# Kernel tuning notes

Hardware: AMD Instinct MI355X
Metric: run time of the kernel (lower is better)

The kernel has to match this reference:

```python
import jax, jax.numpy as jnp
import numpy as np

H = 16
D_MODEL = 1024
D_K = D_MODEL // H


def setup_inputs() -> dict:
    key = jax.random.key(0)
    ks = jax.random.split(key, 11)
    B, S = 4, 2048
    scale = 1.0 / np.sqrt(D_MODEL)
    inp = {
        "query": jax.random.normal(ks[0], (B, S, D_MODEL), dtype=jnp.float32),
        "key": jax.random.normal(ks[1], (B, S, D_MODEL), dtype=jnp.float32),
        "value": jax.random.normal(ks[2], (B, S, D_MODEL), dtype=jnp.float32),
        "Wq": jax.random.normal(ks[3], (D_MODEL, D_MODEL), dtype=jnp.float32) * scale,
        "bq": jnp.zeros((D_MODEL,), dtype=jnp.float32),
        "Wk": jax.random.normal(ks[4], (D_MODEL, D_MODEL), dtype=jnp.float32) * scale,
        "bk": jnp.zeros((D_MODEL,), dtype=jnp.float32),
        "Wv": jax.random.normal(ks[5], (D_MODEL, D_MODEL), dtype=jnp.float32) * scale,
        "bv": jnp.zeros((D_MODEL,), dtype=jnp.float32),
        "Wo": jax.random.normal(ks[6], (D_MODEL, D_MODEL), dtype=jnp.float32) * scale,
        "bo": jnp.zeros((D_MODEL,), dtype=jnp.float32),
    }
    return inp


def reference(query, key, value, Wq, bq, Wk, bk, Wv, bv, Wo, bo):
    B, S, _ = query.shape

    def proj(x, W, b):
        # nn.Linear: x @ W.T + b, then split heads -> [B, H, S, D_K]
        y = jnp.einsum("bsd,ed->bse", x, W) + b
        return y.reshape(B, S, H, D_K).transpose(0, 2, 1, 3)

    q = proj(query, Wq, bq)
    k = proj(key, Wk, bk)
    v = proj(value, Wv, bv)

    scores = jnp.einsum("bhqd,bhkd->bhqk", q, k) / jnp.sqrt(jnp.float32(D_K))
    attn = jax.nn.softmax(scores, axis=-1)
    out = jnp.einsum("bhqk,bhkd->bhqd", attn, v)  # [B,H,S,D_K]
    out = out.transpose(0, 2, 1, 3).reshape(B, S, H * D_K)
    # final linear (dropout disabled in eval / deterministic reference)
    return jnp.einsum("bsd,ed->bse", out, Wo) + bo
```

## Files before the change

kernel.cpp:

```cpp
#include <hip/hip_runtime.h>
#include <stdint.h>

typedef __attribute__((ext_vector_type(8))) short short8;
typedef __attribute__((ext_vector_type(4))) float floatx4;

#define DEV __device__ __forceinline__

DEV unsigned short f2bf(float x) {
  unsigned u = __float_as_uint(x);
  u += 0x7fffu + ((u >> 16) & 1u);
  return (unsigned short)(u >> 16);
}

DEV unsigned pkbf(float hi, float lo) {
  return __builtin_amdgcn_perm(__float_as_uint(hi) + 0x8000u,
                               __float_as_uint(lo) + 0x8000u, 0x07060302u);
}

DEV void load_lds16(const unsigned short* g, unsigned short* l) {
  __builtin_amdgcn_global_load_lds(
      (const __attribute__((address_space(1))) void*)g,
      (__attribute__((address_space(3))) void*)l, 16, 0, 0);
}

DEV void lds_fence() { asm volatile("" ::: "memory"); }

__global__ void cvt_all(const float* __restrict__ Wq, const float* __restrict__ Wk,
                        const float* __restrict__ Wv, const float* __restrict__ Wo,
                        const float* __restrict__ Xq, const float* __restrict__ Xk,
                        const float* __restrict__ Xv,
                        unsigned short* __restrict__ Wb, unsigned short* __restrict__ XqB,
                        unsigned short* __restrict__ XkB, unsigned short* __restrict__ XvB) {
  int bid = blockIdx.x;
  const float* src;
  unsigned short* dst;
  int off;
  if (bid < 4096) {
    int sel = bid >> 10;
    src = sel == 0 ? Wq : sel == 1 ? Wk : sel == 2 ? Wv : Wo;
    dst = Wb + (size_t)sel * 1048576;
    off = bid & 1023;
  } else {
    bid -= 4096;
    int sel = bid >> 13;
    src = sel == 0 ? Xq : sel == 1 ? Xk : Xv;
    dst = sel == 0 ? XqB : sel == 1 ? XkB : XvB;
    off = bid & 8191;
  }
  int i = (off * 256 + threadIdx.x) * 4;
  float4 v = *(const float4*)(src + i);
  uint2 o;
  o.x = pkbf(v.y, v.x);
  o.y = pkbf(v.w, v.z);
  *(uint2*)(dst + i) = o;
}

#define SCQ (0.125f * 1.44269504089f)
__global__ __launch_bounds__(256, 2) void qkv_gemm(
    const unsigned short* __restrict__ XqB, const unsigned short* __restrict__ XkB,
    const unsigned short* __restrict__ XvB,
    const unsigned short* __restrict__ Wb,
    const float* __restrict__ bq, const float* __restrict__ bk, const float* __restrict__ bv,
    unsigned short* __restrict__ Qp, unsigned short* __restrict__ Kp,
    unsigned short* __restrict__ VTp) {
  __shared__ alignas(16) unsigned short Xs[128 * 32];
  __shared__ alignas(16) unsigned short Ws[128 * 32];
  const int z = blockIdx.z;
  const unsigned short* X = z == 0 ? XqB : z == 1 ? XkB : XvB;
  const unsigned short* W = Wb + (size_t)z * 1048576;
  const float* bias = z == 0 ? bq : z == 1 ? bk : bv;

  const int tid = threadIdx.x;
  const int lane = tid & 63, wave = tid >> 6;
  const int lcol = lane & 15, quad = lane >> 4;
  const int wo = blockIdx.x * 128;
  const int xo = blockIdx.y * 128;
  const int wm = (wave & 1) * 64;
  const int wn = (wave >> 1) * 64;

  floatx4 acc[4][4];
  for (int mi = 0; mi < 4; ++mi)
    for (int ni = 0; ni < 4; ++ni)
      for (int r = 0; r < 4; ++r) acc[mi][ni][r] = 0.f;

  const unsigned short* Abuf = (z < 2) ? Xs : Ws;
  const unsigned short* Bbuf = (z < 2) ? Ws : Xs;

  for (int kt = 0; kt < 32; ++kt) {
    const int k0 = kt * 32;
    int c = tid;
    load_lds16(W + (size_t)(wo + (c >> 2)) * 1024 + k0 + (c & 3) * 8, Ws + c * 8);
    load_lds16(X + (size_t)(xo + (c >> 2)) * 1024 + k0 + (c & 3) * 8, Xs + c * 8);
    c = tid + 256;
    load_lds16(W + (size_t)(wo + (c >> 2)) * 1024 + k0 + (c & 3) * 8, Ws + c * 8);
    load_lds16(X + (size_t)(xo + (c >> 2)) * 1024 + k0 + (c & 3) * 8, Xs + c * 8);
    __syncthreads();
    short8 af[4], bf[4];
#pragma unroll
    for (int mi = 0; mi < 4; ++mi)
      af[mi] = *(const short8*)(Abuf + (wm + mi * 16 + lcol) * 32 + quad * 8);
#pragma unroll
    for (int ni = 0; ni < 4; ++ni)
      bf[ni] = *(const short8*)(Bbuf + (wn + ni * 16 + lcol) * 32 + quad * 8);
#pragma unroll
    for (int mi = 0; mi < 4; ++mi)
#pragma unroll
      for (int ni = 0; ni < 4; ++ni)
        acc[mi][ni] = __builtin_amdgcn_mfma_f32_16x16x32_bf16(af[mi], bf[ni], acc[mi][ni], 0, 0, 0);
    __syncthreads();
  }

  if (z < 2) {
    unsigned short* Out = z == 0 ? Qp : Kp;
    const float scl = z == 0 ? SCQ : 1.f;
#pragma unroll
    for (int ni = 0; ni < 4; ++ni) {
      int col = wo + wn + ni * 16 + lcol;
      float bvx = bias[col];
      int h = col >> 6, d = col & 63;
#pragma unroll
      for (int mi = 0; mi < 4; ++mi) {
        int rbase = xo + wm + mi * 16 + quad * 4;
#pragma unroll
        for (int r = 0; r < 4; ++r) {
          int grow = rbase + r;
          int bb = grow >> 11, s = grow & 2047;
          Out[((size_t)(bb * 16 + h) * 2048 + s) * 64 + d] = f2bf((acc[mi][ni][r] + bvx) * scl);
        }
      }
    }
  } else {
#pragma unroll
    for (int mi = 0; mi < 4; ++mi) {
      int dbase = wo + wm + mi * 16 + quad * 4;
#pragma unroll
      for (int r = 0; r < 4; ++r) {
        int dg = dbase + r;
        float bvx = bias[dg];
        int h = dg >> 6, dk = dg & 63;
#pragma unroll
        for (int ni = 0; ni < 4; ++ni) {
          int sg = xo + wn + ni * 16 + lcol;
          int bb = sg >> 11, ss = sg & 2047;
          VTp[((size_t)(bb * 16 + h) * 64 + dk) * 2048 + ss] = f2bf(acc[mi][ni][r] + bvx);
        }
      }
    }
  }
}

__global__ __launch_bounds__(256, 2) void gemm_o(
    const unsigned short* __restrict__ A, const unsigned short* __restrict__ Bw,
    const float* __restrict__ bias, float* __restrict__ Out) {
  __shared__ alignas(16) unsigned short As[128 * 32];
  __shared__ alignas(16) unsigned short Bs[128 * 32];
  const int tid = threadIdx.x;
  const int lane = tid & 63, wave = tid >> 6;
  const int lcol = lane & 15, quad = lane >> 4;
  const int n0 = blockIdx.x * 128;
  const int m0 = blockIdx.y * 128;
  const int wm = (wave & 1) * 64;
  const int wn = (wave >> 1) * 64;

  floatx4 acc[4][4];
  for (int mi = 0; mi < 4; ++mi)
    for (int ni = 0; ni < 4; ++ni)
      for (int r = 0; r < 4; ++r) acc[mi][ni][r] = 0.f;

  for (int kt = 0; kt < 32; ++kt) {
    const int k0 = kt * 32;
    int c = tid;
    load_lds16(Bw + (size_t)(n0 + (c >> 2)) * 1024 + k0 + (c & 3) * 8, Bs + c * 8);
    load_lds16(A  + (size_t)(m0 + (c >> 2)) * 1024 + k0 + (c & 3) * 8, As + c * 8);
    c = tid + 256;
    load_lds16(Bw + (size_t)(n0 + (c >> 2)) * 1024 + k0 + (c & 3) * 8, Bs + c * 8);
    load_lds16(A  + (size_t)(m0 + (c >> 2)) * 1024 + k0 + (c & 3) * 8, As + c * 8);
    __syncthreads();
    short8 af[4], bf[4];
#pragma unroll
    for (int mi = 0; mi < 4; ++mi)
      af[mi] = *(const short8*)(As + (wm + mi * 16 + lcol) * 32 + quad * 8);
#pragma unroll
    for (int ni = 0; ni < 4; ++ni)
      bf[ni] = *(const short8*)(Bs + (wn + ni * 16 + lcol) * 32 + quad * 8);
#pragma unroll
    for (int mi = 0; mi < 4; ++mi)
#pragma unroll
      for (int ni = 0; ni < 4; ++ni)
        acc[mi][ni] = __builtin_amdgcn_mfma_f32_16x16x32_bf16(af[mi], bf[ni], acc[mi][ni], 0, 0, 0);
    __syncthreads();
  }
#pragma unroll
  for (int ni = 0; ni < 4; ++ni) {
    int col = n0 + wn + ni * 16 + lcol;
    float bv = bias[col];
#pragma unroll
    for (int mi = 0; mi < 4; ++mi) {
      int rbase = m0 + wm + mi * 16 + quad * 4;
#pragma unroll
      for (int r = 0; r < 4; ++r)
        Out[(size_t)(rbase + r) * 1024 + col] = acc[mi][ni][r] + bv;
    }
  }
}

__global__ __launch_bounds__(256, 2) void attn_kernel(
    const unsigned short* __restrict__ Qp, const unsigned short* __restrict__ Kp,
    const unsigned short* __restrict__ VTp, unsigned short* __restrict__ Ctx) {
  __shared__ alignas(16) unsigned short Ks[128 * 64];
  __shared__ alignas(16) unsigned short Vt[64 * 128];

  const int tid = threadIdx.x;
  const int lane = tid & 63, wave = tid >> 6;
  const int lcol = lane & 15, quad = lane >> 4;
  const int wq = wave * 32;
  const int qt = blockIdx.x, h = blockIdx.y, b = blockIdx.z;
  const size_t bh = (size_t)(b * 16 + h) * 2048 * 64;
  const unsigned short* Qb = Qp + bh + (size_t)qt * 128 * 64;
  const unsigned short* Kb = Kp + bh;
  const unsigned short* VTb = VTp + (size_t)(b * 16 + h) * 64 * 2048;

#pragma unroll
  for (int i = 0; i < 4; ++i) {
    int p = tid + i * 256;
    int row = p >> 3, pj = p & 7;
    load_lds16(Qb + row * 64 + ((pj ^ (row & 7)) * 8), Ks + p * 8);
  }
  __syncthreads();
  short8 qf[2][2];
#pragma unroll
  for (int ni = 0; ni < 2; ++ni)
#pragma unroll
    for (int ks = 0; ks < 2; ++ks) {
      int row = wq + ni * 16 + lcol;
      qf[ni][ks] = *(const short8*)(Ks + row * 64 + (((ks * 4 + quad) ^ (row & 7)) * 8));
    }

  float M[2] = {-1e30f, -1e30f};
  float L[2] = {0.f, 0.f};
  floatx4 Oacc[2][4];
  for (int mi = 0; mi < 2; ++mi)
    for (int nd = 0; nd < 4; ++nd)
      for (int r = 0; r < 4; ++r) Oacc[mi][nd][r] = 0.f;

  for (int jt = 0; jt < 16; ++jt) {
    __syncthreads();
#pragma unroll
    for (int i = 0; i < 4; ++i) {
      int p = tid + i * 256;
      int kr = p >> 3, kj = p & 7;
      load_lds16(Kb + (size_t)jt * 8192 + kr * 64 + ((kj ^ (kr & 7)) * 8), Ks + p * 8);
      int vr = p >> 4, vj = p & 15;
      load_lds16(VTb + (size_t)vr * 2048 + jt * 128 + ((vj ^ (vr & 7)) * 8), Vt + p * 8);
    }
    __syncthreads();

    floatx4 sacc[8][2];
    for (int mi = 0; mi < 8; ++mi)
      for (int ni = 0; ni < 2; ++ni)
        for (int r = 0; r < 4; ++r) sacc[mi][ni][r] = 0.f;
#pragma unroll
    for (int mi = 0; mi < 8; ++mi) {
      int row = mi * 16 + lcol;
      int sw = (row & 7);
      short8 kf0 = *(const short8*)(Ks + row * 64 + ((quad ^ sw) * 8));
      short8 kf1 = *(const short8*)(Ks + row * 64 + (((4 + quad) ^ sw) * 8));
#pragma unroll
      for (int ni = 0; ni < 2; ++ni) {
        sacc[mi][ni] = __builtin_amdgcn_mfma_f32_16x16x32_bf16(kf0, qf[ni][0], sacc[mi][ni], 0, 0, 0);
        sacc[mi][ni] = __builtin_amdgcn_mfma_f32_16x16x32_bf16(kf1, qf[ni][1], sacc[mi][ni], 0, 0, 0);
      }
    }

    float alpha[2];
#pragma unroll
    for (int ni = 0; ni < 2; ++ni) {
      float mx = -1e30f;
#pragma unroll
      for (int mi = 0; mi < 8; ++mi)
#pragma unroll
        for (int r = 0; r < 4; ++r) mx = fmaxf(mx, sacc[mi][ni][r]);
      mx = fmaxf(mx, __shfl_xor(mx, 16));
      mx = fmaxf(mx, __shfl_xor(mx, 32));
      float mnew = fmaxf(M[ni], mx);
      alpha[ni] = exp2f(M[ni] - mnew);
      M[ni] = mnew;
      float rs = 0.f;
#pragma unroll
      for (int mi = 0; mi < 8; ++mi)
#pragma unroll
        for (int r = 0; r < 4; ++r) {
          float p = exp2f(sacc[mi][ni][r] - mnew);
          sacc[mi][ni][r] = p;
          rs += p;
        }
      rs += __shfl_xor(rs, 16);
      rs += __shfl_xor(rs, 32);
      L[ni] = L[ni] * alpha[ni] + rs;
    }
#pragma unroll
    for (int mi = 0; mi < 2; ++mi)
#pragma unroll
      for (int r = 0; r < 4; ++r) {
        float a = __shfl(alpha[mi], quad * 4 + r);
#pragma unroll
        for (int nd = 0; nd < 4; ++nd) Oacc[mi][nd][r] *= a;
      }

    __syncthreads();

#pragma unroll
    for (int half = 0; half < 2; ++half) {
#pragma unroll
      for (int ni = 0; ni < 2; ++ni) {
        int q = wq + ni * 16 + lcol;
        int sw = q & 7;
#pragma unroll
        for (int m2 = 0; m2 < 4; ++m2) {
          int mi = half * 4 + m2;
          uint2 pw;
          pw.x = pkbf(sacc[mi][ni][1], sacc[mi][ni][0]);
          pw.y = pkbf(sacc[mi][ni][3], sacc[mi][ni][2]);
          int j = 2 * m2 + (quad >> 1);
          *(uint2*)(Ks + q * 64 + ((j ^ sw) * 8) + (quad & 1) * 4) = pw;
        }
      }
      lds_fence();
#pragma unroll
      for (int kk = 0; kk < 2; ++kk) {
        short8 pf[2];
#pragma unroll
        for (int mi = 0; mi < 2; ++mi) {
          int q = wq + mi * 16 + lcol;
          pf[mi] = *(const short8*)(Ks + q * 64 + (((4 * kk + quad) ^ (q & 7)) * 8));
        }
#pragma unroll
        for (int nd = 0; nd < 4; ++nd) {
          int d = nd * 16 + lcol;
          short8 vf = *(const short8*)(Vt + d * 128 + ((((half * 2 + kk) * 4 + quad) ^ (d & 7)) * 8));
#pragma unroll
          for (int mi = 0; mi < 2; ++mi)
            Oacc[mi][nd] = __builtin_amdgcn_mfma_f32_16x16x32_bf16(pf[mi], vf, Oacc[mi][nd], 0, 0, 0);
        }
      }
      lds_fence();
    }
  }

  float linv[2] = {1.f / L[0], 1.f / L[1]};
#pragma unroll
  for (int mi = 0; mi < 2; ++mi)
#pragma unroll
    for (int r = 0; r < 4; ++r) {
      float li = __shfl(linv[mi], quad * 4 + r);
      int q = wq + mi * 16 + quad * 4 + r;
      int sw = q & 7;
#pragma unroll
      for (int nd = 0; nd < 4; ++nd) {
        int j = 2 * nd + (lcol >> 3);
        Ks[q * 64 + ((j ^ sw) * 8) + (lcol & 7)] = f2bf(Oacc[mi][nd][r] * li);
      }
    }
  __syncthreads();
#pragma unroll
  for (int i = 0; i < 4; ++i) {
    int c = tid + i * 256;
    int row = c >> 3, pj = c & 7;
    uint4 v = *(const uint4*)(Ks + row * 64 + ((pj ^ (row & 7)) * 8));
    *(uint4*)(Ctx + ((size_t)(b * 2048 + qt * 128 + row)) * 1024 + h * 64 + pj * 8) = v;
  }
}

extern "C" void kernel_launch(void* const* d_in, const int* in_sizes, int n_in,
                              void* d_out, int out_size, void* d_ws, size_t ws_size,
                              hipStream_t stream) {
  const float* query = (const float*)d_in[0];
  const float* key_  = (const float*)d_in[1];
  const float* value = (const float*)d_in[2];
  const float* Wq = (const float*)d_in[3];
  const float* bq = (const float*)d_in[4];
  const float* Wk = (const float*)d_in[5];
  const float* bk = (const float*)d_in[6];
  const float* Wv = (const float*)d_in[7];
  const float* bv = (const float*)d_in[8];
  const float* Wo = (const float*)d_in[9];
  const float* bo = (const float*)d_in[10];

  char* w = (char*)d_ws;
  unsigned short* Wb  = (unsigned short*)w; w += (size_t)4 * 1024 * 1024 * 2;
  unsigned short* Qp  = (unsigned short*)w; w += (size_t)8192 * 1024 * 2;
  unsigned short* Kp  = (unsigned short*)w; w += (size_t)8192 * 1024 * 2;
  unsigned short* VTp = (unsigned short*)w; w += (size_t)8192 * 1024 * 2;
  unsigned short* Ctx = (unsigned short*)w; w += (size_t)8192 * 1024 * 2;

  unsigned short* XqB = (unsigned short*)d_out;
  unsigned short* XkB = (unsigned short*)d_out + (size_t)8192 * 1024;
  unsigned short* XvB = Ctx;

  cvt_all<<<28672, 256, 0, stream>>>(Wq, Wk, Wv, Wo, query, key_, value,
                                     Wb, XqB, XkB, XvB);

  qkv_gemm<<<dim3(8, 64, 3), 256, 0, stream>>>(XqB, XkB, XvB, Wb,
                                               bq, bk, bv, Qp, Kp, VTp);

  attn_kernel<<<dim3(16, 16, 4), 256, 0, stream>>>(Qp, Kp, VTp, Ctx);

  gemm_o<<<dim3(8, 64), 256, 0, stream>>>(Ctx, Wb + (size_t)3 * 1048576, bo, (float*)d_out);
}
```

Measured before the change: 415.1 us.

## Double-buffer LDS tiles in GEMMs and attention, add lazy softmax rescale

The QKV, output-projection and attention kernels now keep two LDS tile buffers and issue the global-to-LDS loads for the next K tile before computing on the current one. Each iteration therefore needs one barrier instead of two, and load latency can overlap with MFMA work. Attention also gets a separate P/Q buffer, a tree max reduction, and a lazy rescale that skips the alpha multiply while the new row max stays within 8 of the running max. This doubles LDS per block (about 80KB in attention), which may reduce occupancy. The lazy rescale lets exp values grow up to 2^8 before renormalisation.

```diff
diff --git a/kernel.cpp b/kernel.cpp
--- a/kernel.cpp
+++ b/kernel.cpp
@@ -63,8 +63,8 @@
     const float* __restrict__ bq, const float* __restrict__ bk, const float* __restrict__ bv,
     unsigned short* __restrict__ Qp, unsigned short* __restrict__ Kp,
     unsigned short* __restrict__ VTp) {
-  __shared__ alignas(16) unsigned short Xs[128 * 32];
-  __shared__ alignas(16) unsigned short Ws[128 * 32];
+  __shared__ alignas(16) unsigned short Xs[2][128 * 32];
+  __shared__ alignas(16) unsigned short Ws[2][128 * 32];
   const int z = blockIdx.z;
   const unsigned short* X = z == 0 ? XqB : z == 1 ? XkB : XvB;
   const unsigned short* W = Wb + (size_t)z * 1048576;
@@ -83,30 +83,41 @@
     for (int ni = 0; ni < 4; ++ni)
       for (int r = 0; r < 4; ++r) acc[mi][ni][r] = 0.f;
 
-  const unsigned short* Abuf = (z < 2) ? Xs : Ws;
-  const unsigned short* Bbuf = (z < 2) ? Ws : Xs;
+  {
+    int c = tid;
+    load_lds16(W + (size_t)(wo + (c >> 2)) * 1024 + (c & 3) * 8, Ws[0] + c * 8);
+    load_lds16(X + (size_t)(xo + (c >> 2)) * 1024 + (c & 3) * 8, Xs[0] + c * 8);
+    c = tid + 256;
+    load_lds16(W + (size_t)(wo + (c >> 2)) * 1024 + (c & 3) * 8, Ws[0] + c * 8);
+    load_lds16(X + (size_t)(xo + (c >> 2)) * 1024 + (c & 3) * 8, Xs[0] + c * 8);
+  }
+  __syncthreads();
 
   for (int kt = 0; kt < 32; ++kt) {
-    const int k0 = kt * 32;
-    int c = tid;
-    load_lds16(W + (size_t)(wo + (c >> 2)) * 1024 + k0 + (c & 3) * 8, Ws + c * 8);
-    load_lds16(X + (size_t)(xo + (c >> 2)) * 1024 + k0 + (c & 3) * 8, Xs + c * 8);
-    c = tid + 256;
-    load_lds16(W + (size_t)(wo + (c >> 2)) * 1024 + k0 + (c & 3) * 8, Ws + c * 8);
-    load_lds16(X + (size_t)(xo + (c >> 2)) * 1024 + k0 + (c & 3) * 8, Xs + c * 8);
-    __syncthreads();
-    short8 af[4], bf[4];
+    const int cur = kt & 1;
+    if (kt != 31) {
+      const int k0 = (kt + 1) * 32;
+      int c = tid;
+      load_lds16(W + (size_t)(wo + (c >> 2)) * 1024 + k0 + (c & 3) * 8, Ws[cur ^ 1] + c * 8);
+      load_lds16(X + (size_t)(xo + (c >> 2)) * 1024 + k0 + (c & 3) * 8, Xs[cur ^ 1] + c * 8);
+      c = tid + 256;
+      load_lds16(W + (size_t)(wo + (c >> 2)) * 1024 + k0 + (c & 3) * 8, Ws[cur ^ 1] + c * 8);
+      load_lds16(X + (size_t)(xo + (c >> 2)) * 1024 + k0 + (c & 3) * 8, Xs[cur ^ 1] + c * 8);
+    }
+    const unsigned short* Ab = (z < 2) ? Xs[cur] : Ws[cur];
+    const unsigned short* Bb = (z < 2) ? Ws[cur] : Xs[cur];
+    short8 af[4], bfr[4];
 #pragma unroll
     for (int mi = 0; mi < 4; ++mi)
-      af[mi] = *(const short8*)(Abuf + (wm + mi * 16 + lcol) * 32 + quad * 8);
+      af[mi] = *(const short8*)(Ab + (wm + mi * 16 + lcol) * 32 + quad * 8);
 #pragma unroll
     for (int ni = 0; ni < 4; ++ni)
-      bf[ni] = *(const short8*)(Bbuf + (wn + ni * 16 + lcol) * 32 + quad * 8);
+      bfr[ni] = *(const short8*)(Bb + (wn + ni * 16 + lcol) * 32 + quad * 8);
 #pragma unroll
     for (int mi = 0; mi < 4; ++mi)
 #pragma unroll
       for (int ni = 0; ni < 4; ++ni)
-        acc[mi][ni] = __builtin_amdgcn_mfma_f32_16x16x32_bf16(af[mi], bf[ni], acc[mi][ni], 0, 0, 0);
+        acc[mi][ni] = __builtin_amdgcn_mfma_f32_16x16x32_bf16(af[mi], bfr[ni], acc[mi][ni], 0, 0, 0);
     __syncthreads();
   }
 
@@ -152,8 +163,8 @@
 __global__ __launch_bounds__(256, 2) void gemm_o(
     const unsigned short* __restrict__ A, const unsigned short* __restrict__ Bw,
     const float* __restrict__ bias, float* __restrict__ Out) {
-  __shared__ alignas(16) unsigned short As[128 * 32];
-  __shared__ alignas(16) unsigned short Bs[128 * 32];
+  __shared__ alignas(16) unsigned short As[2][128 * 32];
+  __shared__ alignas(16) unsigned short Bs[2][128 * 32];
   const int tid = threadIdx.x;
   const int lane = tid & 63, wave = tid >> 6;
   const int lcol = lane & 15, quad = lane >> 4;
@@ -167,27 +178,39 @@
     for (int ni = 0; ni < 4; ++ni)
       for (int r = 0; r < 4; ++r) acc[mi][ni][r] = 0.f;
 
+  {
+    int c = tid;
+    load_lds16(Bw + (size_t)(n0 + (c >> 2)) * 1024 + (c & 3) * 8, Bs[0] + c * 8);
+    load_lds16(A  + (size_t)(m0 + (c >> 2)) * 1024 + (c & 3) * 8, As[0] + c * 8);
+    c = tid + 256;
+    load_lds16(Bw + (size_t)(n0 + (c >> 2)) * 1024 + (c & 3) * 8, Bs[0] + c * 8);
+    load_lds16(A  + (size_t)(m0 + (c >> 2)) * 1024 + (c & 3) * 8, As[0] + c * 8);
+  }
+  __syncthreads();
+
   for (int kt = 0; kt < 32; ++kt) {
-    const int k0 = kt * 32;
-    int c = tid;
-    load_lds16(Bw + (size_t)(n0 + (c >> 2)) * 1024 + k0 + (c & 3) * 8, Bs + c * 8);
-    load_lds16(A  + (size_t)(m0 + (c >> 2)) * 1024 + k0 + (c & 3) * 8, As + c * 8);
-    c = tid + 256;
-    load_lds16(Bw + (size_t)(n0 + (c >> 2)) * 1024 + k0 + (c & 3) * 8, Bs + c * 8);
-    load_lds16(A  + (size_t)(m0 + (c >> 2)) * 1024 + k0 + (c & 3) * 8, As + c * 8);
-    __syncthreads();
-    short8 af[4], bf[4];
+    const int cur = kt & 1;
+    if (kt != 31) {
+      const int k0 = (kt + 1) * 32;
+      int c = tid;
+      load_lds16(Bw + (size_t)(n0 + (c >> 2)) * 1024 + k0 + (c & 3) * 8, Bs[cur ^ 1] + c * 8);
+      load_lds16(A  + (size_t)(m0 + (c >> 2)) * 1024 + k0 + (c & 3) * 8, As[cur ^ 1] + c * 8);
+      c = tid + 256;
+      load_lds16(Bw + (size_t)(n0 + (c >> 2)) * 1024 + k0 + (c & 3) * 8, Bs[cur ^ 1] + c * 8);
+      load_lds16(A  + (size_t)(m0 + (c >> 2)) * 1024 + k0 + (c & 3) * 8, As[cur ^ 1] + c * 8);
+    }
+    short8 af[4], bfr[4];
 #pragma unroll
     for (int mi = 0; mi < 4; ++mi)
-      af[mi] = *(const short8*)(As + (wm + mi * 16 + lcol) * 32 + quad * 8);
+      af[mi] = *(const short8*)(As[cur] + (wm + mi * 16 + lcol) * 32 + quad * 8);
 #pragma unroll
     for (int ni = 0; ni < 4; ++ni)
-      bf[ni] = *(const short8*)(Bs + (wn + ni * 16 + lcol) * 32 + quad * 8);
+      bfr[ni] = *(const short8*)(Bs[cur] + (wn + ni * 16 + lcol) * 32 + quad * 8);
 #pragma unroll
     for (int mi = 0; mi < 4; ++mi)
 #pragma unroll
       for (int ni = 0; ni < 4; ++ni)
-        acc[mi][ni] = __builtin_amdgcn_mfma_f32_16x16x32_bf16(af[mi], bf[ni], acc[mi][ni], 0, 0, 0);
+        acc[mi][ni] = __builtin_amdgcn_mfma_f32_16x16x32_bf16(af[mi], bfr[ni], acc[mi][ni], 0, 0, 0);
     __syncthreads();
   }
 #pragma unroll
@@ -207,8 +230,9 @@
 __global__ __launch_bounds__(256, 2) void attn_kernel(
     const unsigned short* __restrict__ Qp, const unsigned short* __restrict__ Kp,
     const unsigned short* __restrict__ VTp, unsigned short* __restrict__ Ctx) {
-  __shared__ alignas(16) unsigned short Ks[128 * 64];
-  __shared__ alignas(16) unsigned short Vt[64 * 128];
+  __shared__ alignas(16) unsigned short Ks[2][128 * 64];
+  __shared__ alignas(16) unsigned short Vt[2][64 * 128];
+  __shared__ alignas(16) unsigned short Ps[128 * 64];
 
   const int tid = threadIdx.x;
   const int lane = tid & 63, wave = tid >> 6;
@@ -224,16 +248,25 @@
   for (int i = 0; i < 4; ++i) {
     int p = tid + i * 256;
     int row = p >> 3, pj = p & 7;
-    load_lds16(Qb + row * 64 + ((pj ^ (row & 7)) * 8), Ks + p * 8);
+    load_lds16(Qb + row * 64 + ((pj ^ (row & 7)) * 8), Ps + p * 8);
+  }
+#pragma unroll
+  for (int i = 0; i < 4; ++i) {
+    int p = tid + i * 256;
+    int kr = p >> 3, kj = p & 7;
+    load_lds16(Kb + kr * 64 + ((kj ^ (kr & 7)) * 8), Ks[0] + p * 8);
+    int vr = p >> 4, vj = p & 15;
+    load_lds16(VTb + (size_t)vr * 2048 + ((vj ^ (vr & 7)) * 8), Vt[0] + p * 8);
   }
   __syncthreads();
+
   short8 qf[2][2];
 #pragma unroll
   for (int ni = 0; ni < 2; ++ni)
 #pragma unroll
     for (int ks = 0; ks < 2; ++ks) {
       int row = wq + ni * 16 + lcol;
-      qf[ni][ks] = *(const short8*)(Ks + row * 64 + (((ks * 4 + quad) ^ (row & 7)) * 8));
+      qf[ni][ks] = *(const short8*)(Ps + row * 64 + (((ks * 4 + quad) ^ (row & 7)) * 8));
     }
 
   float M[2] = {-1e30f, -1e30f};
@@ -244,17 +277,21 @@
       for (int r = 0; r < 4; ++r) Oacc[mi][nd][r] = 0.f;
 
   for (int jt = 0; jt < 16; ++jt) {
-    __syncthreads();
-#pragma unroll
-    for (int i = 0; i < 4; ++i) {
-      int p = tid + i * 256;
-      int kr = p >> 3, kj = p & 7;
-      load_lds16(Kb + (size_t)jt * 8192 + kr * 64 + ((kj ^ (kr & 7)) * 8), Ks + p * 8);
-      int vr = p >> 4, vj = p & 15;
-      load_lds16(VTb + (size_t)vr * 2048 + jt * 128 + ((vj ^ (vr & 7)) * 8), Vt + p * 8);
-    }
-    __syncthreads();
-
+    const int cur = jt & 1;
+    if (jt != 15) {
+#pragma unroll
+      for (int i = 0; i < 4; ++i) {
+        int p = tid + i * 256;
+        int kr = p >> 3, kj = p & 7;
+        load_lds16(Kb + (size_t)(jt + 1) * 8192 + kr * 64 + ((kj ^ (kr & 7)) * 8),
+                   Ks[cur ^ 1] + p * 8);
+        int vr = p >> 4, vj = p & 15;
+        load_lds16(VTb + (size_t)vr * 2048 + (jt + 1) * 128 + ((vj ^ (vr & 7)) * 8),
+                   Vt[cur ^ 1] + p * 8);
+      }
+    }
+
+    const unsigned short* Kc = Ks[cur];
     floatx4 sacc[8][2];
     for (int mi = 0; mi < 8; ++mi)
       for (int ni = 0; ni < 2; ++ni)
@@ -263,8 +300,8 @@
     for (int mi = 0; mi < 8; ++mi) {
       int row = mi * 16 + lcol;
       int sw = (row & 7);
-      short8 kf0 = *(const short8*)(Ks + row * 64 + ((quad ^ sw) * 8));
-      short8 kf1 = *(const short8*)(Ks + row * 64 + (((4 + quad) ^ sw) * 8));
+      short8 kf0 = *(const short8*)(Kc + row * 64 + ((quad ^ sw) * 8));
+      short8 kf1 = *(const short8*)(Kc + row * 64 + (((4 + quad) ^ sw) * 8));
 #pragma unroll
       for (int ni = 0; ni < 2; ++ni) {
         sacc[mi][ni] = __builtin_amdgcn_mfma_f32_16x16x32_bf16(kf0, qf[ni][0], sacc[mi][ni], 0, 0, 0);
@@ -272,43 +309,59 @@
       }
     }
 
-    float alpha[2];
+    float mx[2];
 #pragma unroll
     for (int ni = 0; ni < 2; ++ni) {
-      float mx = -1e30f;
+      float pm[8];
 #pragma unroll
       for (int mi = 0; mi < 8; ++mi)
-#pragma unroll
-        for (int r = 0; r < 4; ++r) mx = fmaxf(mx, sacc[mi][ni][r]);
-      mx = fmaxf(mx, __shfl_xor(mx, 16));
-      mx = fmaxf(mx, __shfl_xor(mx, 32));
-      float mnew = fmaxf(M[ni], mx);
-      alpha[ni] = exp2f(M[ni] - mnew);
-      M[ni] = mnew;
-      float rs = 0.f;
-#pragma unroll
-      for (int mi = 0; mi < 8; ++mi)
+        pm[mi] = fmaxf(fmaxf(sacc[mi][ni][0], sacc[mi][ni][1]),
+                       fmaxf(sacc[mi][ni][2], sacc[mi][ni][3]));
+      float t0 = fmaxf(fmaxf(pm[0], pm[1]), fmaxf(pm[2], pm[3]));
+      float t1 = fmaxf(fmaxf(pm[4], pm[5]), fmaxf(pm[6], pm[7]));
+      float m = fmaxf(t0, t1);
+      m = fmaxf(m, __shfl_xor(m, 16));
+      m = fmaxf(m, __shfl_xor(m, 32));
+      mx[ni] = m;
+    }
+    const int skip = __all((mx[0] <= M[0] + 8.f) & (mx[1] <= M[1] + 8.f));
+    float alpha[2] = {1.f, 1.f};
+    if (!skip) {
+#pragma unroll
+      for (int ni = 0; ni < 2; ++ni) {
+        float mnew = fmaxf(M[ni], mx[ni]);
+        alpha[ni] = exp2f(M[ni] - mnew);
+        M[ni] = mnew;
+      }
+#pragma unroll
+      for (int mi = 0; mi < 2; ++mi)
 #pragma unroll
         for (int r = 0; r < 4; ++r) {
-          float p = exp2f(sacc[mi][ni][r] - mnew);
-          sacc[mi][ni][r] = p;
-          rs += p;
-        }
+          float a = __shfl(alpha[mi], quad * 4 + r);
+          floatx4 av = {a, a, a, a};
+#pragma unroll
+          for (int nd = 0; nd < 4; ++nd) Oacc[mi][nd] *= av;
+        }
+    }
+#pragma unroll
+    for (int ni = 0; ni < 2; ++ni) {
+      floatx4 mv = {M[ni], M[ni], M[ni], M[ni]};
+      floatx4 rv = {0.f, 0.f, 0.f, 0.f};
+#pragma unroll
+      for (int mi = 0; mi < 8; ++mi) {
+        floatx4 t = sacc[mi][ni] - mv;
+        floatx4 p;
+        p[0] = exp2f(t[0]); p[1] = exp2f(t[1]); p[2] = exp2f(t[2]); p[3] = exp2f(t[3]);
+        sacc[mi][ni] = p;
+        rv += p;
+      }
+      float rs = (rv[0] + rv[1]) + (rv[2] + rv[3]);
       rs += __shfl_xor(rs, 16);
       rs += __shfl_xor(rs, 32);
-      L[ni] = L[ni] * alpha[ni] + rs;
-    }
-#pragma unroll
-    for (int mi = 0; mi < 2; ++mi)
-#pragma unroll
-      for (int r = 0; r < 4; ++r) {
-        float a = __shfl(alpha[mi], quad * 4 + r);
-#pragma unroll
-        for (int nd = 0; nd < 4; ++nd) Oacc[mi][nd][r] *= a;
-      }
-
-    __syncthreads();
-
+      L[ni] = skip ? (L[ni] + rs) : (L[ni] * alpha[ni] + rs);
+    }
+
+    const unsigned short* Vc = Vt[cur];
 #pragma unroll
     for (int half = 0; half < 2; ++half) {
 #pragma unroll
@@ -322,7 +375,7 @@
           pw.x = pkbf(sacc[mi][ni][1], sacc[mi][ni][0]);
           pw.y = pkbf(sacc[mi][ni][3], sacc[mi][ni][2]);
           int j = 2 * m2 + (quad >> 1);
-          *(uint2*)(Ks + q * 64 + ((j ^ sw) * 8) + (quad & 1) * 4) = pw;
+          *(uint2*)(Ps + q * 64 + ((j ^ sw) * 8) + (quad & 1) * 4) = pw;
         }
       }
       lds_fence();
@@ -332,12 +385,12 @@
 #pragma unroll
         for (int mi = 0; mi < 2; ++mi) {
           int q = wq + mi * 16 + lcol;
-          pf[mi] = *(const short8*)(Ks + q * 64 + (((4 * kk + quad) ^ (q & 7)) * 8));
+          pf[mi] = *(const short8*)(Ps + q * 64 + (((4 * kk + quad) ^ (q & 7)) * 8));
         }
 #pragma unroll
         for (int nd = 0; nd < 4; ++nd) {
           int d = nd * 16 + lcol;
-          short8 vf = *(const short8*)(Vt + d * 128 + ((((half * 2 + kk) * 4 + quad) ^ (d & 7)) * 8));
+          short8 vf = *(const short8*)(Vc + d * 128 + ((((half * 2 + kk) * 4 + quad) ^ (d & 7)) * 8));
 #pragma unroll
           for (int mi = 0; mi < 2; ++mi)
             Oacc[mi][nd] = __builtin_amdgcn_mfma_f32_16x16x32_bf16(pf[mi], vf, Oacc[mi][nd], 0, 0, 0);
@@ -345,6 +398,7 @@
       }
       lds_fence();
     }
+    __syncthreads();
   }
 
   float linv[2] = {1.f / L[0], 1.f / L[1]};
@@ -358,7 +412,7 @@
 #pragma unroll
       for (int nd = 0; nd < 4; ++nd) {
         int j = 2 * nd + (lcol >> 3);
-        Ks[q * 64 + ((j ^ sw) * 8) + (lcol & 7)] = f2bf(Oacc[mi][nd][r] * li);
+        Ps[q * 64 + ((j ^ sw) * 8) + (lcol & 7)] = f2bf(Oacc[mi][nd][r] * li);
       }
     }
   __syncthreads();
@@ -366,7 +420,7 @@
   for (int i = 0; i < 4; ++i) {
     int c = tid + i * 256;
     int row = c >> 3, pj = c & 7;
-    uint4 v = *(const uint4*)(Ks + row * 64 + ((pj ^ (row & 7)) * 8));
+    uint4 v = *(const uint4*)(Ps + row * 64 + ((pj ^ (row & 7)) * 8));
     *(uint4*)(Ctx + ((size_t)(b * 2048 + qt * 128 + row)) * 1024 + h * 64 + pj * 8) = v;
   }
 }
```

New measurement: 414.2 us. About the same (-0.2%).
